# Kernel optimization log

Hardware: AMD Instinct MI355X
Metric: run time of the kernel (lower is better)

## Reference

```python
import jax, jax.numpy as jnp
import numpy as np

N_NODES = 100000
N_EDGES = 1600000
N_GRAPHS = 128
IN_F, H_F, OUT_F, HID, NCLS = 128, 128, 64, 10, 10

def setup_inputs() -> dict:
    key = jax.random.key(0)
    ks = jax.random.split(key, 12)
    feats = jax.random.normal(ks[0], (N_NODES, IN_F), dtype=jnp.float32)
    src = jax.random.randint(ks[1], (N_EDGES,), 0, N_NODES, dtype=jnp.int32)
    dst = jax.random.randint(ks[2], (N_EDGES,), 0, N_NODES, dtype=jnp.int32)
    graph_ids = jnp.sort(jax.random.randint(ks[3], (N_NODES,), 0, N_GRAPHS, dtype=jnp.int32))
    def glorot(k, shape):
        fan = shape[0] + shape[1]
        return jax.random.normal(k, shape, dtype=jnp.float32) * jnp.sqrt(2.0 / fan)
    return {
        'feats': feats, 'src': src, 'dst': dst, 'graph_ids': graph_ids,
        'W1': glorot(ks[4], (IN_F, H_F)), 'b1': jnp.zeros((H_F,), jnp.float32),
        'W2': glorot(ks[5], (H_F, OUT_F)), 'b2': jnp.zeros((OUT_F,), jnp.float32),
        'fcW1': glorot(ks[6], (OUT_F, HID)), 'fcb1': jnp.zeros((HID,), jnp.float32),
        'fcW2': glorot(ks[7], (HID, NCLS)), 'fcb2': jnp.zeros((NCLS,), jnp.float32),
    }

def _graph_conv(x, W, b, src, dst):
    # DGL GraphConv, norm='both': D_dst^{-1/2} A D_src^{-1/2} X W + b
    ones = jnp.ones((src.shape[0],), x.dtype)
    deg_out = jnp.clip(jax.ops.segment_sum(ones, src, num_segments=N_NODES), 1.0)
    deg_in = jnp.clip(jax.ops.segment_sum(ones, dst, num_segments=N_NODES), 1.0)
    x = x * jax.lax.rsqrt(deg_out)[:, None]
    m = jax.ops.segment_sum(x[src], dst, num_segments=N_NODES)  # gather-scatter over edges
    m = m * jax.lax.rsqrt(deg_in)[:, None]
    return m @ W + b

def reference(feats, src, dst, graph_ids, W1, b1, W2, b2, fcW1, fcb1, fcW2, fcb2):
    h = jax.nn.relu(_graph_conv(feats, W1, b1, src, dst))
    h = jax.nn.relu(_graph_conv(h, W2, b2, src, dst))
    # dgl.mean_nodes: per-graph mean pooling
    sums = jax.ops.segment_sum(h, graph_ids, num_segments=N_GRAPHS)
    counts = jnp.clip(jax.ops.segment_sum(jnp.ones((N_NODES,), h.dtype), graph_ids, num_segments=N_GRAPHS), 1.0)
    pooled = sums / counts[:, None]  # [G, OUT_F]
    z = jax.nn.relu(pooled @ fcW1 + fcb1)
    return jax.nn.softmax(z @ fcW2 + fcb2, axis=1)
```

## Files before the change

kernel.cpp:

```cpp
#include <hip/hip_runtime.h>
#include <hip/hip_bf16.h>

#define N_NODES 100000
#define N_EDGES 1600000
#define N_GRAPHS 128
#define IN_F 128
#define H_F 128
#define OUT_F 64
#define HID 10
#define NCLS 10
#define XPAD 136
#define BSH 7
#define NBUCK 782
#define SBLK 128
#define EPB (N_EDGES / SBLK)
#define NB_PREP 4
#define PCHUNK 8

typedef __attribute__((ext_vector_type(8))) short bf16x8;
typedef __attribute__((ext_vector_type(4))) float f32x4;
typedef __attribute__((ext_vector_type(2))) float f32x2;

__device__ __forceinline__ float bl(unsigned int u) { return __uint_as_float(u << 16); }
__device__ __forceinline__ float bh(unsigned int u) { return __uint_as_float(u & 0xffff0000u); }

__global__ __launch_bounds__(1024) void k_hist2(const int* __restrict__ src, const int* __restrict__ dst,
                                                int* __restrict__ Pd, int* __restrict__ Ps,
                                                const float* __restrict__ W1, const float* __restrict__ W2,
                                                unsigned short* __restrict__ Wt1, unsigned short* __restrict__ Wt2) {
    __shared__ int hd[NBUCK];
    __shared__ int hs[NBUCK];
    const int blk = blockIdx.x;
    if (blk < SBLK) {
        for (int i = threadIdx.x; i < NBUCK; i += 1024) { hd[i] = 0; hs[i] = 0; }
        __syncthreads();
        const int base = blk * EPB;
        for (int i = threadIdx.x; i < EPB; i += 1024) {
            atomicAdd(&hd[dst[base + i] >> BSH], 1);
            atomicAdd(&hs[src[base + i] >> BSH], 1);
        }
        __syncthreads();
        for (int b = threadIdx.x; b < NBUCK; b += 1024) {
            Pd[b * SBLK + blk] = hd[b];
            Ps[b * SBLK + blk] = hs[b];
        }
    } else {
        int t = (blk - SBLK) * 1024 + threadIdx.x;
        const int stride = NB_PREP * 1024;
        for (int i = t; i < 128 * 128; i += stride) {
            int c = i >> 7, k = i & 127;
            __hip_bfloat16 v = __float2bfloat16(W1[k * 128 + c]);
            Wt1[i] = *(unsigned short*)&v;
        }
        for (int i = t; i < 64 * 128; i += stride) {
            int c = i >> 7, k = i & 127;
            __hip_bfloat16 v = __float2bfloat16(W2[k * 64 + c]);
            Wt2[i] = *(unsigned short*)&v;
        }
    }
}

__global__ __launch_bounds__(128) void k_scanA(int* __restrict__ Pd, int* __restrict__ Ps,
                                               int* __restrict__ Td, int* __restrict__ Ts) {
    __shared__ int sc[128];
    const int b = blockIdx.x;
    const int t = threadIdx.x;
    int* P = (b < NBUCK) ? Pd : Ps;
    int* T = (b < NBUCK) ? Td : Ts;
    const int bb = (b < NBUCK) ? b : b - NBUCK;
    int v = P[bb * SBLK + t];
    sc[t] = v;
    __syncthreads();
    for (int off = 1; off < 128; off <<= 1) {
        int u = (t >= off) ? sc[t - off] : 0;
        __syncthreads();
        sc[t] += u;
        __syncthreads();
    }
    P[bb * SBLK + t] = sc[t] - v;
    if (t == 127) T[bb] = sc[127];
}

__global__ __launch_bounds__(1024) void k_scanB(const int* __restrict__ Td, const int* __restrict__ Ts,
                                                int* __restrict__ Bd, int* __restrict__ Bs) {
    __shared__ int sc[1024];
    const int t = threadIdx.x;
    int v = (t < NBUCK) ? Td[t] : 0;
    sc[t] = v;
    __syncthreads();
    for (int off = 1; off < 1024; off <<= 1) {
        int u = (t >= off) ? sc[t - off] : 0;
        __syncthreads();
        sc[t] += u;
        __syncthreads();
    }
    if (t < NBUCK) Bd[t] = sc[t] - v;
    if (t == NBUCK - 1) Bd[NBUCK] = sc[t];
    __syncthreads();
    int v2 = (t < NBUCK) ? Ts[t] : 0;
    sc[t] = v2;
    __syncthreads();
    for (int off = 1; off < 1024; off <<= 1) {
        int u = (t >= off) ? sc[t - off] : 0;
        __syncthreads();
        sc[t] += u;
        __syncthreads();
    }
    if (t < NBUCK) Bs[t] = sc[t] - v2;
    if (t == NBUCK - 1) Bs[NBUCK] = sc[t];
}

__global__ __launch_bounds__(1024) void k_scatter(const int* __restrict__ src, const int* __restrict__ dst,
                                                  const int* __restrict__ Pd, const int* __restrict__ Ps,
                                                  const int* __restrict__ Bd, const int* __restrict__ Bs,
                                                  unsigned int* __restrict__ pb, unsigned char* __restrict__ sb) {
    __shared__ int tk[NBUCK];
    const int b = blockIdx.x;
    const bool isPb = b < SBLK;
    const int blk = isPb ? b : b - SBLK;
    for (int i = threadIdx.x; i < NBUCK; i += 1024) tk[i] = 0;
    __syncthreads();
    const int base = blk * EPB;
    if (isPb) {
        for (int i = threadIdx.x; i < EPB; i += 1024) {
            int d = dst[base + i];
            int s = src[base + i];
            int bd = d >> BSH;
            int t = atomicAdd(&tk[bd], 1);
            pb[Bd[bd] + Pd[bd * SBLK + blk] + t] = ((unsigned)s << 7) | (unsigned)(d & 127);
        }
    } else {
        for (int i = threadIdx.x; i < EPB; i += 1024) {
            int s = src[base + i];
            int bs = s >> BSH;
            int t = atomicAdd(&tk[bs], 1);
            sb[Bs[bs] + Ps[bs * SBLK + blk] + t] = (unsigned char)(s & 127);
        }
    }
}

__global__ __launch_bounds__(256) void k_finalize(const unsigned int* __restrict__ pb, const int* __restrict__ Bd,
                                                  const unsigned char* __restrict__ sb, const int* __restrict__ Bs,
                                                  int* __restrict__ rp, int* __restrict__ cnt_out,
                                                  int* __restrict__ cols) {
    __shared__ int cnt[128];
    __shared__ int exc[128];
    __shared__ int tick[128];
    __shared__ int h[128];
    __shared__ int sc[128];
    const int b = blockIdx.x;
    const int tid = threadIdx.x;
    if (tid < 128) { cnt[tid] = 0; tick[tid] = 0; h[tid] = 0; }
    __syncthreads();
    const int e0 = Bd[b], e1 = Bd[b + 1];
    for (int i = e0 + tid; i < e1; i += 256) atomicAdd(&cnt[pb[i] & 127], 1);
    const int f0 = Bs[b], f1 = Bs[b + 1];
    for (int i = f0 + tid; i < f1; i += 256) atomicAdd(&h[sb[i]], 1);
    __syncthreads();
    if (tid < 128) sc[tid] = cnt[tid];
    __syncthreads();
    for (int off = 1; off < 128; off <<= 1) {
        int u = (tid < 128 && tid >= off) ? sc[tid - off] : 0;
        __syncthreads();
        if (tid < 128) sc[tid] += u;
        __syncthreads();
    }
    if (tid < 128) exc[tid] = sc[tid] - cnt[tid];
    __syncthreads();
    const int node0 = b << BSH;
    if (tid < 128 && node0 + tid < N_NODES) {
        rp[node0 + tid] = e0 + exc[tid];
        cnt_out[node0 + tid] = h[tid];
    }
    if (b == NBUCK - 1 && tid == 0) rp[N_NODES] = N_EDGES;
    for (int i = e0 + tid; i < e1; i += 256) {
        unsigned int p = pb[i];
        int loc = p & 127;
        int t = atomicAdd(&tick[loc], 1);
        cols[e0 + exc[loc] + t] = (int)(p >> 7);
    }
}

__global__ __launch_bounds__(256) void k_gemm1(const float* __restrict__ X,
                                               const unsigned short* __restrict__ Wt,
                                               const int* __restrict__ cnt_out,
                                               unsigned char* __restrict__ Gout) {
    __shared__ __align__(16) unsigned short Xs[32 * XPAD];
    __shared__ __align__(16) unsigned short Ws[128 * XPAD];
    const int tid = threadIdx.x;
    const int row0 = blockIdx.x * 32;

    {
        const float4* X4 = (const float4*)X;
#pragma unroll
        for (int j = 0; j < 4; j++) {
            int i = tid + 256 * j;
            int r = i >> 5, k4 = i & 31;
            float4 x = X4[(size_t)(row0 + r) * 32 + k4];
            __hip_bfloat162 lo = __float22bfloat162_rn({x.x, x.y});
            __hip_bfloat162 hi = __float22bfloat162_rn({x.z, x.w});
            uint2 u;
            u.x = *(unsigned int*)&lo;
            u.y = *(unsigned int*)&hi;
            *(uint2*)&Xs[r * XPAD + k4 * 4] = u;
        }
    }
    {
        const uint2* W2 = (const uint2*)Wt;
#pragma unroll
        for (int j = 0; j < 16; j++) {
            int i = tid + 256 * j;
            int cc = i >> 5, kk = i & 31;
            uint2 u = W2[(size_t)cc * 32 + kk];
            *(uint2*)&Ws[cc * XPAD + kk * 4] = u;
        }
    }
    __syncthreads();

    const int lane = tid & 63;
    const int wv = tid >> 6;
    const int m = lane & 15;
    const int q = lane >> 4;
    const int cg = wv * 32;

    f32x4 acc00 = {0.f, 0.f, 0.f, 0.f}, acc01 = {0.f, 0.f, 0.f, 0.f};
    f32x4 acc10 = {0.f, 0.f, 0.f, 0.f}, acc11 = {0.f, 0.f, 0.f, 0.f};
#pragma unroll
    for (int ks = 0; ks < 4; ks++) {
        int kb = ks * 32 + q * 8;
        bf16x8 a0 = *(const bf16x8*)&Xs[m * XPAD + kb];
        bf16x8 a1 = *(const bf16x8*)&Xs[(16 + m) * XPAD + kb];
        bf16x8 b0 = *(const bf16x8*)&Ws[(cg + m) * XPAD + kb];
        bf16x8 b1 = *(const bf16x8*)&Ws[(cg + 16 + m) * XPAD + kb];
        acc00 = __builtin_amdgcn_mfma_f32_16x16x32_bf16(a0, b0, acc00, 0, 0, 0);
        acc01 = __builtin_amdgcn_mfma_f32_16x16x32_bf16(a0, b1, acc01, 0, 0, 0);
        acc10 = __builtin_amdgcn_mfma_f32_16x16x32_bf16(a1, b0, acc10, 0, 0, 0);
        acc11 = __builtin_amdgcn_mfma_f32_16x16x32_bf16(a1, b1, acc11, 0, 0, 0);
    }
#pragma unroll
    for (int r = 0; r < 4; r++) {
        int rowA = row0 + q * 4 + r;
        int rowB = rowA + 16;
        float sA = rsqrtf((float)max(cnt_out[rowA], 1));
        float sB = rsqrtf((float)max(cnt_out[rowB], 1));
        unsigned int pkA = __builtin_amdgcn_cvt_pk_fp8_f32(acc00[r] * sA, acc01[r] * sA, 0, false);
        unsigned int pkB = __builtin_amdgcn_cvt_pk_fp8_f32(acc10[r] * sB, acc11[r] * sB, 0, false);
        unsigned char* gA = Gout + (size_t)rowA * 128 + cg + m;
        gA[0]  = (unsigned char)(pkA & 0xffu);
        gA[16] = (unsigned char)((pkA >> 8) & 0xffu);
        unsigned char* gB = Gout + (size_t)rowB * 128 + cg + m;
        gB[0]  = (unsigned char)(pkB & 0xffu);
        gB[16] = (unsigned char)((pkB >> 8) & 0xffu);
    }
}

template <int TOTF, bool XBF16, bool OUT_FP8>
__global__ __launch_bounds__(256) void k_gemm_mfma(const void* __restrict__ Xv,
                                                   const unsigned short* __restrict__ Wt,
                                                   const int* __restrict__ cnt_out,
                                                   void* __restrict__ GoutV) {
    __shared__ __align__(16) unsigned short Xs[32 * XPAD];
    __shared__ __align__(16) unsigned short Ws[64 * XPAD];
    const int tid = threadIdx.x;
    const int cbase = blockIdx.y * 64;
    const int row0 = blockIdx.x * 32;

    if constexpr (XBF16) {
        const uint2* X2 = (const uint2*)Xv;
#pragma unroll
        for (int j = 0; j < 4; j++) {
            int i = tid + 256 * j;
            int r = i >> 5, kk = i & 31;
            uint2 u = X2[(size_t)(row0 + r) * 32 + kk];
            *(uint2*)&Xs[r * XPAD + kk * 4] = u;
        }
    } else {
        const float4* X4 = (const float4*)Xv;
#pragma unroll
        for (int j = 0; j < 4; j++) {
            int i = tid + 256 * j;
            int r = i >> 5, k4 = i & 31;
            float4 x = X4[(size_t)(row0 + r) * 32 + k4];
            __hip_bfloat162 lo = __float22bfloat162_rn({x.x, x.y});
            __hip_bfloat162 hi = __float22bfloat162_rn({x.z, x.w});
            uint2 u;
            u.x = *(unsigned int*)&lo;
            u.y = *(unsigned int*)&hi;
            *(uint2*)&Xs[r * XPAD + k4 * 4] = u;
        }
    }
    {
        const uint2* W2 = (const uint2*)Wt;
#pragma unroll
        for (int j = 0; j < 8; j++) {
            int i = tid + 256 * j;
            int c = i >> 5, kk = i & 31;
            uint2 u = W2[(size_t)(cbase + c) * 32 + kk];
            *(uint2*)&Ws[c * XPAD + kk * 4] = u;
        }
    }
    __syncthreads();

    const int lane = tid & 63;
    const int wv = tid >> 6;
    const int m = lane & 15;
    const int q = lane >> 4;
    const int roff = (wv & 1) * 16;
    const int coff = (wv >> 1) * 32;

    f32x4 acc0 = {0.f, 0.f, 0.f, 0.f}, acc1 = {0.f, 0.f, 0.f, 0.f};
#pragma unroll
    for (int ks = 0; ks < 4; ks++) {
        int kb = ks * 32 + q * 8;
        bf16x8 a  = *(const bf16x8*)&Xs[(roff + m) * XPAD + kb];
        bf16x8 b0 = *(const bf16x8*)&Ws[(coff + m) * XPAD + kb];
        bf16x8 b1 = *(const bf16x8*)&Ws[(coff + 16 + m) * XPAD + kb];
        acc0 = __builtin_amdgcn_mfma_f32_16x16x32_bf16(a, b0, acc0, 0, 0, 0);
        acc1 = __builtin_amdgcn_mfma_f32_16x16x32_bf16(a, b1, acc1, 0, 0, 0);
    }
#pragma unroll
    for (int r = 0; r < 4; r++) {
        int row = row0 + roff + q * 4 + r;
        float s = rsqrtf((float)max(cnt_out[row], 1));
        int col0 = cbase + coff + m;
        if constexpr (OUT_FP8) {
            unsigned int pk = __builtin_amdgcn_cvt_pk_fp8_f32(acc0[r] * s, acc1[r] * s, 0, false);
            unsigned char* gp = (unsigned char*)GoutV + (size_t)row * TOTF + col0;
            gp[0]  = (unsigned char)(pk & 0xffu);
            gp[16] = (unsigned char)((pk >> 8) & 0xffu);
        } else {
            unsigned short* Gout = (unsigned short*)GoutV;
            __hip_bfloat16 o0 = __float2bfloat16(acc0[r] * s);
            __hip_bfloat16 o1 = __float2bfloat16(acc1[r] * s);
            Gout[(size_t)row * TOTF + col0]      = *(unsigned short*)&o0;
            Gout[(size_t)row * TOTF + col0 + 16] = *(unsigned short*)&o1;
        }
    }
}

__device__ __forceinline__ void acc8(uint2 u, f32x2& a01, f32x2& a23, f32x2& a45, f32x2& a67) {
    a01 += __builtin_amdgcn_cvt_pk_f32_fp8(u.x, false);
    a23 += __builtin_amdgcn_cvt_pk_f32_fp8(u.x, true);
    a45 += __builtin_amdgcn_cvt_pk_f32_fp8(u.y, false);
    a67 += __builtin_amdgcn_cvt_pk_f32_fp8(u.y, true);
}
__device__ __forceinline__ float red2(float x) {
    x += __shfl_xor(x, 16);
    x += __shfl_xor(x, 32);
    return x;
}

__global__ __launch_bounds__(256) void k_spmm128f8(const unsigned int* __restrict__ G,
                                                   const int* __restrict__ rp,
                                                   const int* __restrict__ cols,
                                                   const float* __restrict__ bias,
                                                   uint4* __restrict__ H4) {
    const int lane = threadIdx.x & 63;
    const int wave = threadIdx.x >> 6;
    const int v = blockIdx.x * 4 + wave;
    const int b0 = rp[v];
    const int deg = rp[v + 1] - b0;
    const int c = lane & 15;
    const int h = lane >> 4;
    const uint2* G2 = (const uint2*)G;
    f32x2 a01 = {0.f, 0.f}, a23 = {0.f, 0.f}, a45 = {0.f, 0.f}, a67 = {0.f, 0.f};
    for (int base = 0; base < deg; base += 64) {
        const int n = min(64, deg - base);
        const int mycol = (lane < n) ? cols[b0 + base + lane] : 0;
        const int n16 = n & ~15;
        for (int j = 0; j < n16; j += 16) {
            int s0 = __shfl(mycol, j + h);
            int s1 = __shfl(mycol, j + 4 + h);
            int s2 = __shfl(mycol, j + 8 + h);
            int s3 = __shfl(mycol, j + 12 + h);
            uint2 u0 = G2[(size_t)s0 * 16 + c];
            uint2 u1 = G2[(size_t)s1 * 16 + c];
            uint2 u2 = G2[(size_t)s2 * 16 + c];
            uint2 u3 = G2[(size_t)s3 * 16 + c];
            acc8(u0, a01, a23, a45, a67);
            acc8(u1, a01, a23, a45, a67);
            acc8(u2, a01, a23, a45, a67);
            acc8(u3, a01, a23, a45, a67);
        }
        for (int j = n16; j < n; j += 4) {
            int idx = j + h;
            int sj = __shfl(mycol, min(idx, n - 1));
            if (idx < n) {
                uint2 u = G2[(size_t)sj * 16 + c];
                acc8(u, a01, a23, a45, a67);
            }
        }
    }
    float r0 = red2(a01.x), r1 = red2(a01.y), r2 = red2(a23.x), r3 = red2(a23.y);
    float r4 = red2(a45.x), r5 = red2(a45.y), r6 = red2(a67.x), r7 = red2(a67.y);
    if (h == 0) {
        float rs = rsqrtf((float)max(deg, 1));
        float4 bA = *(const float4*)&bias[8 * c];
        float4 bB = *(const float4*)&bias[8 * c + 4];
        __hip_bfloat162 p0 = __float22bfloat162_rn({fmaxf(fmaf(r0, rs, bA.x), 0.f),
                                                    fmaxf(fmaf(r1, rs, bA.y), 0.f)});
        __hip_bfloat162 p1 = __float22bfloat162_rn({fmaxf(fmaf(r2, rs, bA.z), 0.f),
                                                    fmaxf(fmaf(r3, rs, bA.w), 0.f)});
        __hip_bfloat162 p2 = __float22bfloat162_rn({fmaxf(fmaf(r4, rs, bB.x), 0.f),
                                                    fmaxf(fmaf(r5, rs, bB.y), 0.f)});
        __hip_bfloat162 p3 = __float22bfloat162_rn({fmaxf(fmaf(r6, rs, bB.z), 0.f),
                                                    fmaxf(fmaf(r7, rs, bB.w), 0.f)});
        uint4 o;
        o.x = *(unsigned int*)&p0;
        o.y = *(unsigned int*)&p1;
        o.z = *(unsigned int*)&p2;
        o.w = *(unsigned int*)&p3;
        H4[(size_t)v * 16 + c] = o;
    }
}

__global__ __launch_bounds__(256) void k_spmm64f8(const unsigned int* __restrict__ G,
                                                  const int* __restrict__ rp,
                                                  const int* __restrict__ cols,
                                                  const float* __restrict__ bias,
                                                  uint2* __restrict__ H2) {
    const int lane = threadIdx.x & 63;
    const int wave = threadIdx.x >> 6;
    const int v = blockIdx.x * 4 + wave;
    const int b0 = rp[v];
    const int deg = rp[v + 1] - b0;
    const int c = lane & 15;
    const int h = lane >> 4;
    f32x2 a01 = {0.f, 0.f}, a23 = {0.f, 0.f};
    for (int base = 0; base < deg; base += 64) {
        const int n = min(64, deg - base);
        const int mycol = (lane < n) ? cols[b0 + base + lane] : 0;
        const int n16 = n & ~15;
        for (int j = 0; j < n16; j += 16) {
            int s0 = __shfl(mycol, j + h);
            int s1 = __shfl(mycol, j + 4 + h);
            int s2 = __shfl(mycol, j + 8 + h);
            int s3 = __shfl(mycol, j + 12 + h);
            unsigned int u0 = G[(size_t)s0 * 16 + c];
            unsigned int u1 = G[(size_t)s1 * 16 + c];
            unsigned int u2 = G[(size_t)s2 * 16 + c];
            unsigned int u3 = G[(size_t)s3 * 16 + c];
            a01 += __builtin_amdgcn_cvt_pk_f32_fp8(u0, false);
            a23 += __builtin_amdgcn_cvt_pk_f32_fp8(u0, true);
            a01 += __builtin_amdgcn_cvt_pk_f32_fp8(u1, false);
            a23 += __builtin_amdgcn_cvt_pk_f32_fp8(u1, true);
            a01 += __builtin_amdgcn_cvt_pk_f32_fp8(u2, false);
            a23 += __builtin_amdgcn_cvt_pk_f32_fp8(u2, true);
            a01 += __builtin_amdgcn_cvt_pk_f32_fp8(u3, false);
            a23 += __builtin_amdgcn_cvt_pk_f32_fp8(u3, true);
        }
        for (int j = n16; j < n; j += 4) {
            int idx = j + h;
            int sj = __shfl(mycol, min(idx, n - 1));
            if (idx < n) {
                unsigned int u = G[(size_t)sj * 16 + c];
                a01 += __builtin_amdgcn_cvt_pk_f32_fp8(u, false);
                a23 += __builtin_amdgcn_cvt_pk_f32_fp8(u, true);
            }
        }
    }
    float ax = red2(a01.x), ay = red2(a01.y), az = red2(a23.x), aw = red2(a23.y);
    if (h == 0) {
        float r = rsqrtf((float)max(deg, 1));
        float4 b = *(const float4*)&bias[4 * c];
        __hip_bfloat162 p0 = __float22bfloat162_rn({fmaxf(fmaf(ax, r, b.x), 0.f),
                                                    fmaxf(fmaf(ay, r, b.y), 0.f)});
        __hip_bfloat162 p1 = __float22bfloat162_rn({fmaxf(fmaf(az, r, b.z), 0.f),
                                                    fmaxf(fmaf(aw, r, b.w), 0.f)});
        uint2 o;
        o.x = *(unsigned int*)&p0;
        o.y = *(unsigned int*)&p1;
        H2[(size_t)v * 16 + c] = o;
    }
}

__global__ __launch_bounds__(256) void k_pool(const unsigned short* __restrict__ h2,
                                              const int* __restrict__ gid,
                                              float* __restrict__ part) {
    __shared__ int se[2];
    __shared__ float red[16][16][4];
    const int cpart = blockIdx.x;
    const int g = blockIdx.y;
    const int tid = threadIdx.x;
    if (tid < 2) {
        int target = g + tid;
        int lo = 0, hi = N_NODES;
        while (lo < hi) {
            int mid = (lo + hi) >> 1;
            if (gid[mid] < target) lo = mid + 1; else hi = mid;
        }
        se[tid] = lo;
    }
    __syncthreads();
    const int s = se[0], e = se[1];
    const int chunk = (e - s + PCHUNK - 1) / PCHUNK;
    const int lo = s + cpart * chunk;
    const int hi = min(lo + chunk, e);
    const int r = tid >> 4, cp = tid & 15;
    float a0 = 0.f, a1 = 0.f, a2 = 0.f, a3 = 0.f;
    const uint2* H = (const uint2*)h2;
    for (int v = lo + r; v < hi; v += 16) {
        uint2 u = H[(size_t)v * 16 + cp];
        a0 += bl(u.x); a1 += bh(u.x); a2 += bl(u.y); a3 += bh(u.y);
    }
    red[r][cp][0] = a0; red[r][cp][1] = a1; red[r][cp][2] = a2; red[r][cp][3] = a3;
    for (int off = 8; off > 0; off >>= 1) {
        __syncthreads();
        if (r < off) {
#pragma unroll
            for (int k = 0; k < 4; k++) red[r][cp][k] += red[r + off][cp][k];
        }
    }
    __syncthreads();
    if (r == 0) {
        float4 o = {red[0][cp][0], red[0][cp][1], red[0][cp][2], red[0][cp][3]};
        *(float4*)&part[((size_t)cpart * N_GRAPHS + g) * 64 + 4 * cp] = o;
    }
}

__global__ __launch_bounds__(64) void k_mlp(const float* __restrict__ part,
                                            const int* __restrict__ gid,
                                            const float* __restrict__ fcW1,
                                            const float* __restrict__ fcb1,
                                            const float* __restrict__ fcW2,
                                            const float* __restrict__ fcb2,
                                            float* __restrict__ out) {
    __shared__ int se[2];
    __shared__ float p[64];
    __shared__ float z[10];
    __shared__ float l[10];
    __shared__ float red[2];
    const int g = blockIdx.x;
    const int t = threadIdx.x;
    if (t < 2) {
        int target = g + t;
        int lo = 0, hi = N_NODES;
        while (lo < hi) {
            int mid = (lo + hi) >> 1;
            if (gid[mid] < target) lo = mid + 1; else hi = mid;
        }
        se[t] = lo;
    }
    __syncthreads();
    const int cnt = max(se[1] - se[0], 1);
    float a = 0.f;
#pragma unroll
    for (int c = 0; c < PCHUNK; c++) a += part[((size_t)c * N_GRAPHS + g) * 64 + t];
    p[t] = a / (float)cnt;
    __syncthreads();
    if (t < 10) {
        float acc = fcb1[t];
        for (int k = 0; k < 64; k++) acc = fmaf(p[k], fcW1[k * 10 + t], acc);
        z[t] = fmaxf(acc, 0.f);
    }
    __syncthreads();
    if (t < 10) {
        float acc = fcb2[t];
        for (int k = 0; k < 10; k++) acc = fmaf(z[k], fcW2[k * 10 + t], acc);
        l[t] = acc;
    }
    __syncthreads();
    if (t == 0) {
        float m = l[0];
        for (int i = 1; i < 10; i++) m = fmaxf(m, l[i]);
        float ssum = 0.f;
        for (int i = 0; i < 10; i++) ssum += expf(l[i] - m);
        red[0] = m;
        red[1] = ssum;
    }
    __syncthreads();
    if (t < 10) out[g * 10 + t] = expf(l[t] - red[0]) / red[1];
}

extern "C" void kernel_launch(void* const* d_in, const int* in_sizes, int n_in,
                              void* d_out, int out_size, void* d_ws, size_t ws_size,
                              hipStream_t stream) {
    const float* feats = (const float*)d_in[0];
    const int* src = (const int*)d_in[1];
    const int* dst = (const int*)d_in[2];
    const int* gid = (const int*)d_in[3];
    const float* W1 = (const float*)d_in[4];
    const float* b1 = (const float*)d_in[5];
    const float* W2 = (const float*)d_in[6];
    const float* b2 = (const float*)d_in[7];
    const float* fcW1 = (const float*)d_in[8];
    const float* fcb1 = (const float*)d_in[9];
    const float* fcW2 = (const float*)d_in[10];
    const float* fcb2 = (const float*)d_in[11];
    float* out = (float*)d_out;

    char* w = (char*)d_ws;
    size_t off = 0;
    auto alloc = [&](size_t bytes) -> void* {
        void* p = w + off;
        off = (off + bytes + 255) & ~(size_t)255;
        return p;
    };
    int* cnt_out = (int*)alloc(N_NODES * 4);
    int* rp      = (int*)alloc((N_NODES + 1) * 4);
    int* cols    = (int*)alloc((size_t)N_EDGES * 4);
    int* Pd      = (int*)alloc(NBUCK * SBLK * 4);
    int* Ps      = (int*)alloc(NBUCK * SBLK * 4);
    int* Td      = (int*)alloc(NBUCK * 4);
    int* Ts      = (int*)alloc(NBUCK * 4);
    int* Bd      = (int*)alloc((NBUCK + 1) * 4);
    int* Bs      = (int*)alloc((NBUCK + 1) * 4);
    unsigned int* pb  = (unsigned int*)alloc((size_t)N_EDGES * 4);
    unsigned char* sb = (unsigned char*)alloc((size_t)N_EDGES);
    unsigned short* Wt1 = (unsigned short*)alloc(128 * 128 * 2);
    unsigned short* Wt2 = (unsigned short*)alloc(64 * 128 * 2);
    unsigned char* g1 = (unsigned char*)alloc((size_t)N_NODES * 128);
    unsigned short* h1 = (unsigned short*)alloc((size_t)N_NODES * 128 * 2);
    unsigned char* g2 = (unsigned char*)alloc((size_t)N_NODES * 64);
    unsigned short* h2 = (unsigned short*)alloc((size_t)N_NODES * 64 * 2);
    float* part = (float*)alloc((size_t)PCHUNK * N_GRAPHS * 64 * 4);

    k_hist2<<<SBLK + NB_PREP, 1024, 0, stream>>>(src, dst, Pd, Ps, W1, W2, Wt1, Wt2);
    k_scanA<<<2 * NBUCK, 128, 0, stream>>>(Pd, Ps, Td, Ts);
    k_scanB<<<1, 1024, 0, stream>>>(Td, Ts, Bd, Bs);
    k_scatter<<<2 * SBLK, 1024, 0, stream>>>(src, dst, Pd, Ps, Bd, Bs, pb, sb);
    k_finalize<<<NBUCK, 256, 0, stream>>>(pb, Bd, sb, Bs, rp, cnt_out, cols);

    k_gemm1<<<N_NODES / 32, 256, 0, stream>>>(feats, Wt1, cnt_out, g1);
    k_spmm128f8<<<N_NODES / 4, 256, 0, stream>>>((const unsigned int*)g1, rp, cols, b1, (uint4*)h1);

    k_gemm_mfma<64, true, true><<<dim3(N_NODES / 32, 1), 256, 0, stream>>>(h1, Wt2, cnt_out, g2);
    k_spmm64f8<<<N_NODES / 4, 256, 0, stream>>>((const unsigned int*)g2, rp, cols, b2, (uint2*)h2);

    k_pool<<<dim3(PCHUNK, N_GRAPHS), 256, 0, stream>>>(h2, gid, part);
    k_mlp<<<N_GRAPHS, 64, 0, stream>>>(part, gid, fcW1, fcb1, fcW2, fcb2, out);
}
```

Baseline: 287.9 us.

## Process eight nodes per wave in SpMM with double-buffered neighbor gathers

```diff
diff --git a/kernel.cpp b/kernel.cpp
--- a/kernel.cpp
+++ b/kernel.cpp
@@ -344,35 +344,62 @@
     a45 += __builtin_amdgcn_cvt_pk_f32_fp8(u.y, false);
     a67 += __builtin_amdgcn_cvt_pk_f32_fp8(u.y, true);
 }
+__device__ __forceinline__ void acc4(unsigned int u, f32x2& a01, f32x2& a23) {
+    a01 += __builtin_amdgcn_cvt_pk_f32_fp8(u, false);
+    a23 += __builtin_amdgcn_cvt_pk_f32_fp8(u, true);
+}
 __device__ __forceinline__ float red2(float x) {
     x += __shfl_xor(x, 16);
     x += __shfl_xor(x, 32);
     return x;
 }
 
-__global__ __launch_bounds__(256) void k_spmm128f8(const unsigned int* __restrict__ G,
-                                                   const int* __restrict__ rp,
-                                                   const int* __restrict__ cols,
-                                                   const float* __restrict__ bias,
-                                                   uint4* __restrict__ H4) {
-    const int lane = threadIdx.x & 63;
-    const int wave = threadIdx.x >> 6;
-    const int v = blockIdx.x * 4 + wave;
-    const int b0 = rp[v];
-    const int deg = rp[v + 1] - b0;
-    const int c = lane & 15;
-    const int h = lane >> 4;
-    const uint2* G2 = (const uint2*)G;
-    f32x2 a01 = {0.f, 0.f}, a23 = {0.f, 0.f}, a45 = {0.f, 0.f}, a67 = {0.f, 0.f};
-    for (int base = 0; base < deg; base += 64) {
-        const int n = min(64, deg - base);
-        const int mycol = (lane < n) ? cols[b0 + base + lane] : 0;
-        const int n16 = n & ~15;
+
+__device__ __forceinline__ void gat128(const uint2* __restrict__ G2, int mycol, int nr, int c, int h,
+                                       uint2 (&u)[8]) {
+#pragma unroll
+    for (int s = 0; s < 8; s++)
+        if (4 * s < nr) {
+            int row = __shfl(mycol, 4 * s + h);
+            u[s] = G2[(size_t)row * 16 + c];
+        }
+}
+__device__ __forceinline__ void acc128(const uint2 (&u)[8], int nr, int h,
+                                       f32x2& a01, f32x2& a23, f32x2& a45, f32x2& a67) {
+#pragma unroll
+    for (int s = 0; s < 8; s++) {
+        if (4 * s + 4 <= nr) {
+            acc8(u[s], a01, a23, a45, a67);
+        } else if (4 * s < nr) {
+            bool ok = (4 * s + h) < nr;
+            uint2 uu;
+            uu.x = ok ? u[s].x : 0u;
+            uu.y = ok ? u[s].y : 0u;
+            acc8(uu, a01, a23, a45, a67);
+        }
+    }
+}
+__device__ __forceinline__ void slow128(const uint2* __restrict__ G2, const int* __restrict__ cols,
+                                        int b0, int d, int mycol, int lane, int c, int h,
+                                        f32x2& a01, f32x2& a23, f32x2& a45, f32x2& a67) {
+    const int n = min(d, 64);
+    for (int j = 32; j < n; j += 4) {
+        int idx = j + h;
+        int sj = __shfl(mycol, min(idx, n - 1));
+        if (idx < n) {
+            uint2 uu = G2[(size_t)sj * 16 + c];
+            acc8(uu, a01, a23, a45, a67);
+        }
+    }
+    for (int base = 64; base < d; base += 64) {
+        const int nn = min(64, d - base);
+        const int mc2 = (lane < nn) ? cols[b0 + base + lane] : 0;
+        const int n16 = nn & ~15;
         for (int j = 0; j < n16; j += 16) {
-            int s0 = __shfl(mycol, j + h);
-            int s1 = __shfl(mycol, j + 4 + h);
-            int s2 = __shfl(mycol, j + 8 + h);
-            int s3 = __shfl(mycol, j + 12 + h);
+            int s0 = __shfl(mc2, j + h);
+            int s1 = __shfl(mc2, j + 4 + h);
+            int s2 = __shfl(mc2, j + 8 + h);
+            int s3 = __shfl(mc2, j + 12 + h);
             uint2 u0 = G2[(size_t)s0 * 16 + c];
             uint2 u1 = G2[(size_t)s1 * 16 + c];
             uint2 u2 = G2[(size_t)s2 * 16 + c];
@@ -382,15 +409,19 @@
             acc8(u2, a01, a23, a45, a67);
             acc8(u3, a01, a23, a45, a67);
         }
-        for (int j = n16; j < n; j += 4) {
+        for (int j = n16; j < nn; j += 4) {
             int idx = j + h;
-            int sj = __shfl(mycol, min(idx, n - 1));
-            if (idx < n) {
-                uint2 u = G2[(size_t)sj * 16 + c];
-                acc8(u, a01, a23, a45, a67);
+            int sj = __shfl(mc2, min(idx, nn - 1));
+            if (idx < nn) {
+                uint2 uu = G2[(size_t)sj * 16 + c];
+                acc8(uu, a01, a23, a45, a67);
             }
         }
     }
+}
+__device__ __forceinline__ void store128(uint4* __restrict__ H4, const float* __restrict__ bias,
+                                         int v, int deg, int c, int h,
+                                         f32x2 a01, f32x2 a23, f32x2 a45, f32x2 a67) {
     float r0 = red2(a01.x), r1 = red2(a01.y), r2 = red2(a23.x), r3 = red2(a23.y);
     float r4 = red2(a45.x), r5 = red2(a45.y), r6 = red2(a67.x), r7 = red2(a67.y);
     if (h == 0) {
@@ -414,6 +445,131 @@
     }
 }
 
+__global__ __launch_bounds__(256) void k_spmm128f8(const unsigned int* __restrict__ G,
+                                                   const int* __restrict__ rp,
+                                                   const int* __restrict__ cols,
+                                                   const float* __restrict__ bias,
+                                                   uint4* __restrict__ H4) {
+    const int lane = threadIdx.x & 63;
+    const int wave = threadIdx.x >> 6;
+    const int v0 = (blockIdx.x * 4 + wave) * 8;
+    const int c = lane & 15;
+    const int h = lane >> 4;
+    const uint2* G2 = (const uint2*)G;
+
+    int rpl = (lane < 9) ? rp[v0 + lane] : 0;
+    int rv[9];
+#pragma unroll
+    for (int t = 0; t < 9; t++) rv[t] = __builtin_amdgcn_readfirstlane(__shfl(rpl, t));
+    int b[8], d[8];
+#pragma unroll
+    for (int i = 0; i < 8; i++) { b[i] = rv[i]; d[i] = rv[i + 1] - rv[i]; }
+
+    uint2 u[2][2][8];
+    int mc[2][2];
+    mc[0][0] = (lane < d[0]) ? cols[b[0] + lane] : 0;
+    mc[0][1] = (lane < d[1]) ? cols[b[1] + lane] : 0;
+    mc[1][0] = (lane < d[2]) ? cols[b[2] + lane] : 0;
+    mc[1][1] = (lane < d[3]) ? cols[b[3] + lane] : 0;
+    gat128(G2, mc[0][0], min(d[0], 32), c, h, u[0][0]);
+    gat128(G2, mc[0][1], min(d[1], 32), c, h, u[0][1]);
+
+#pragma unroll
+    for (int p = 0; p < 4; p++) {
+        const int par = p & 1, nxt = par ^ 1;
+        const int i0 = 2 * p, i1 = 2 * p + 1;
+        if (p < 3) {
+            gat128(G2, mc[nxt][0], min(d[i0 + 2], 32), c, h, u[nxt][0]);
+            gat128(G2, mc[nxt][1], min(d[i0 + 3], 32), c, h, u[nxt][1]);
+        }
+        f32x2 a01 = {0.f, 0.f}, a23 = {0.f, 0.f}, a45 = {0.f, 0.f}, a67 = {0.f, 0.f};
+        acc128(u[par][0], min(d[i0], 32), h, a01, a23, a45, a67);
+        if (d[i0] > 32) slow128(G2, cols, b[i0], d[i0], mc[par][0], lane, c, h, a01, a23, a45, a67);
+        f32x2 c01 = {0.f, 0.f}, c23 = {0.f, 0.f}, c45 = {0.f, 0.f}, c67 = {0.f, 0.f};
+        acc128(u[par][1], min(d[i1], 32), h, c01, c23, c45, c67);
+        if (d[i1] > 32) slow128(G2, cols, b[i1], d[i1], mc[par][1], lane, c, h, c01, c23, c45, c67);
+        if (p < 2) {
+            mc[par][0] = (lane < d[i0 + 4]) ? cols[b[i0 + 4] + lane] : 0;
+            mc[par][1] = (lane < d[i0 + 5]) ? cols[b[i0 + 5] + lane] : 0;
+        }
+        store128(H4, bias, v0 + i0, d[i0], c, h, a01, a23, a45, a67);
+        store128(H4, bias, v0 + i1, d[i1], c, h, c01, c23, c45, c67);
+    }
+}
+
+
+__device__ __forceinline__ void gat64(const unsigned int* __restrict__ G, int mycol, int nr, int c, int h,
+                                      unsigned int (&u)[8]) {
+#pragma unroll
+    for (int s = 0; s < 8; s++)
+        if (4 * s < nr) {
+            int row = __shfl(mycol, 4 * s + h);
+            u[s] = G[(size_t)row * 16 + c];
+        }
+}
+__device__ __forceinline__ void acc64s(const unsigned int (&u)[8], int nr, int h,
+                                       f32x2& a01, f32x2& a23) {
+#pragma unroll
+    for (int s = 0; s < 8; s++) {
+        if (4 * s + 4 <= nr) {
+            acc4(u[s], a01, a23);
+        } else if (4 * s < nr) {
+            bool ok = (4 * s + h) < nr;
+            acc4(ok ? u[s] : 0u, a01, a23);
+        }
+    }
+}
+__device__ __forceinline__ void slow64(const unsigned int* __restrict__ G, const int* __restrict__ cols,
+                                       int b0, int d, int mycol, int lane, int c, int h,
+                                       f32x2& a01, f32x2& a23) {
+    const int n = min(d, 64);
+    for (int j = 32; j < n; j += 4) {
+        int idx = j + h;
+        int sj = __shfl(mycol, min(idx, n - 1));
+        if (idx < n) acc4(G[(size_t)sj * 16 + c], a01, a23);
+    }
+    for (int base = 64; base < d; base += 64) {
+        const int nn = min(64, d - base);
+        const int mc2 = (lane < nn) ? cols[b0 + base + lane] : 0;
+        const int n16 = nn & ~15;
+        for (int j = 0; j < n16; j += 16) {
+            int s0 = __shfl(mc2, j + h);
+            int s1 = __shfl(mc2, j + 4 + h);
+            int s2 = __shfl(mc2, j + 8 + h);
+            int s3 = __shfl(mc2, j + 12 + h);
+            unsigned int u0 = G[(size_t)s0 * 16 + c];
+            unsigned int u1 = G[(size_t)s1 * 16 + c];
+            unsigned int u2 = G[(size_t)s2 * 16 + c];
+            unsigned int u3 = G[(size_t)s3 * 16 + c];
+            acc4(u0, a01, a23);
+            acc4(u1, a01, a23);
+            acc4(u2, a01, a23);
+            acc4(u3, a01, a23);
+        }
+        for (int j = n16; j < nn; j += 4) {
+            int idx = j + h;
+            int sj = __shfl(mc2, min(idx, nn - 1));
+            if (idx < nn) acc4(G[(size_t)sj * 16 + c], a01, a23);
+        }
+    }
+}
+__device__ __forceinline__ void store64(uint2* __restrict__ H2, const float* __restrict__ bias,
+                                        int v, int deg, int c, int h, f32x2 a01, f32x2 a23) {
+    float ax = red2(a01.x), ay = red2(a01.y), az = red2(a23.x), aw = red2(a23.y);
+    if (h == 0) {
+        float r = rsqrtf((float)max(deg, 1));
+        float4 bb = *(const float4*)&bias[4 * c];
+        __hip_bfloat162 p0 = __float22bfloat162_rn({fmaxf(fmaf(ax, r, bb.x), 0.f),
+                                                    fmaxf(fmaf(ay, r, bb.y), 0.f)});
+        __hip_bfloat162 p1 = __float22bfloat162_rn({fmaxf(fmaf(az, r, bb.z), 0.f),
+                                                    fmaxf(fmaf(aw, r, bb.w), 0.f)});
+        uint2 o;
+        o.x = *(unsigned int*)&p0;
+        o.y = *(unsigned int*)&p1;
+        H2[(size_t)v * 16 + c] = o;
+    }
+}
+
 __global__ __launch_bounds__(256) void k_spmm64f8(const unsigned int* __restrict__ G,
                                                   const int* __restrict__ rp,
                                                   const int* __restrict__ cols,
@@ -421,56 +577,47 @@
                                                   uint2* __restrict__ H2) {
     const int lane = threadIdx.x & 63;
     const int wave = threadIdx.x >> 6;
-    const int v = blockIdx.x * 4 + wave;
-    const int b0 = rp[v];
-    const int deg = rp[v + 1] - b0;
+    const int v0 = (blockIdx.x * 4 + wave) * 8;
     const int c = lane & 15;
     const int h = lane >> 4;
-    f32x2 a01 = {0.f, 0.f}, a23 = {0.f, 0.f};
-    for (int base = 0; base < deg; base += 64) {
-        const int n = min(64, deg - base);
-        const int mycol = (lane < n) ? cols[b0 + base + lane] : 0;
-        const int n16 = n & ~15;
-        for (int j = 0; j < n16; j += 16) {
-            int s0 = __shfl(mycol, j + h);
-            int s1 = __shfl(mycol, j + 4 + h);
-            int s2 = __shfl(mycol, j + 8 + h);
-            int s3 = __shfl(mycol, j + 12 + h);
-            unsigned int u0 = G[(size_t)s0 * 16 + c];
-            unsigned int u1 = G[(size_t)s1 * 16 + c];
-            unsigned int u2 = G[(size_t)s2 * 16 + c];
-            unsigned int u3 = G[(size_t)s3 * 16 + c];
-            a01 += __builtin_amdgcn_cvt_pk_f32_fp8(u0, false);
-            a23 += __builtin_amdgcn_cvt_pk_f32_fp8(u0, true);
-            a01 += __builtin_amdgcn_cvt_pk_f32_fp8(u1, false);
-            a23 += __builtin_amdgcn_cvt_pk_f32_fp8(u1, true);
-            a01 += __builtin_amdgcn_cvt_pk_f32_fp8(u2, false);
-            a23 += __builtin_amdgcn_cvt_pk_f32_fp8(u2, true);
-            a01 += __builtin_amdgcn_cvt_pk_f32_fp8(u3, false);
-            a23 += __builtin_amdgcn_cvt_pk_f32_fp8(u3, true);
-        }
-        for (int j = n16; j < n; j += 4) {
-            int idx = j + h;
-            int sj = __shfl(mycol, min(idx, n - 1));
-            if (idx < n) {
-                unsigned int u = G[(size_t)sj * 16 + c];
-                a01 += __builtin_amdgcn_cvt_pk_f32_fp8(u, false);
-                a23 += __builtin_amdgcn_cvt_pk_f32_fp8(u, true);
-            }
-        }
-    }
-    float ax = red2(a01.x), ay = red2(a01.y), az = red2(a23.x), aw = red2(a23.y);
-    if (h == 0) {
-        float r = rsqrtf((float)max(deg, 1));
-        float4 b = *(const float4*)&bias[4 * c];
-        __hip_bfloat162 p0 = __float22bfloat162_rn({fmaxf(fmaf(ax, r, b.x), 0.f),
-                                                    fmaxf(fmaf(ay, r, b.y), 0.f)});
-        __hip_bfloat162 p1 = __float22bfloat162_rn({fmaxf(fmaf(az, r, b.z), 0.f),
-                                                    fmaxf(fmaf(aw, r, b.w), 0.f)});
-        uint2 o;
-        o.x = *(unsigned int*)&p0;
-        o.y = *(unsigned int*)&p1;
-        H2[(size_t)v * 16 + c] = o;
+
+    int rpl = (lane < 9) ? rp[v0 + lane] : 0;
+    int rv[9];
+#pragma unroll
+    for (int t = 0; t < 9; t++) rv[t] = __builtin_amdgcn_readfirstlane(__shfl(rpl, t));
+    int b[8], d[8];
+#pragma unroll
+    for (int i = 0; i < 8; i++) { b[i] = rv[i]; d[i] = rv[i + 1] - rv[i]; }
+
+    unsigned int u[2][2][8];
+    int mc[2][2];
+    mc[0][0] = (lane < d[0]) ? cols[b[0] + lane] : 0;
+    mc[0][1] = (lane < d[1]) ? cols[b[1] + lane] : 0;
+    mc[1][0] = (lane < d[2]) ? cols[b[2] + lane] : 0;
+    mc[1][1] = (lane < d[3]) ? cols[b[3] + lane] : 0;
+    gat64(G, mc[0][0], min(d[0], 32), c, h, u[0][0]);
+    gat64(G, mc[0][1], min(d[1], 32), c, h, u[0][1]);
+
+#pragma unroll
+    for (int p = 0; p < 4; p++) {
+        const int par = p & 1, nxt = par ^ 1;
+        const int i0 = 2 * p, i1 = 2 * p + 1;
+        if (p < 3) {
+            gat64(G, mc[nxt][0], min(d[i0 + 2], 32), c, h, u[nxt][0]);
+            gat64(G, mc[nxt][1], min(d[i0 + 3], 32), c, h, u[nxt][1]);
+        }
+        f32x2 a01 = {0.f, 0.f}, a23 = {0.f, 0.f};
+        acc64s(u[par][0], min(d[i0], 32), h, a01, a23);
+        if (d[i0] > 32) slow64(G, cols, b[i0], d[i0], mc[par][0], lane, c, h, a01, a23);
+        f32x2 c01 = {0.f, 0.f}, c23 = {0.f, 0.f};
+        acc64s(u[par][1], min(d[i1], 32), h, c01, c23);
+        if (d[i1] > 32) slow64(G, cols, b[i1], d[i1], mc[par][1], lane, c, h, c01, c23);
+        if (p < 2) {
+            mc[par][0] = (lane < d[i0 + 4]) ? cols[b[i0 + 4] + lane] : 0;
+            mc[par][1] = (lane < d[i0 + 5]) ? cols[b[i0 + 5] + lane] : 0;
+        }
+        store64(H2, bias, v0 + i0, d[i0], c, h, a01, a23);
+        store64(H2, bias, v0 + i1, d[i1], c, h, c01, c23);
     }
 }
 
@@ -622,10 +769,10 @@
     k_finalize<<<NBUCK, 256, 0, stream>>>(pb, Bd, sb, Bs, rp, cnt_out, cols);
 
     k_gemm1<<<N_NODES / 32, 256, 0, stream>>>(feats, Wt1, cnt_out, g1);
-    k_spmm128f8<<<N_NODES / 4, 256, 0, stream>>>((const unsigned int*)g1, rp, cols, b1, (uint4*)h1);
+    k_spmm128f8<<<N_NODES / 32, 256, 0, stream>>>((const unsigned int*)g1, rp, cols, b1, (uint4*)h1);
 
     k_gemm_mfma<64, true, true><<<dim3(N_NODES / 32, 1), 256, 0, stream>>>(h1, Wt2, cnt_out, g2);
-    k_spmm64f8<<<N_NODES / 4, 256, 0, stream>>>((const unsigned int*)g2, rp, cols, b2, (uint2*)h2);
+    k_spmm64f8<<<N_NODES / 32, 256, 0, stream>>>((const unsigned int*)g2, rp, cols, b2, (uint2*)h2);
 
     k_pool<<<dim3(PCHUNK, N_GRAPHS), 256, 0, stream>>>(h2, gid, part);
     k_mlp<<<N_GRAPHS, 64, 0, stream>>>(part, gid, fcW1, fcb1, fcW2, fcb2, out);
```

Result: slower. 333.5 us (+15.8%).

## Remap SpMM gathers so each wave walks edges serially across all feature lanes

Applied to the files above, without the earlier changes.

```diff
diff --git a/kernel.cpp b/kernel.cpp
--- a/kernel.cpp
+++ b/kernel.cpp
@@ -338,140 +338,125 @@
     }
 }
 
-__device__ __forceinline__ void acc8(uint2 u, f32x2& a01, f32x2& a23, f32x2& a45, f32x2& a67) {
-    a01 += __builtin_amdgcn_cvt_pk_f32_fp8(u.x, false);
-    a23 += __builtin_amdgcn_cvt_pk_f32_fp8(u.x, true);
-    a45 += __builtin_amdgcn_cvt_pk_f32_fp8(u.y, false);
-    a67 += __builtin_amdgcn_cvt_pk_f32_fp8(u.y, true);
-}
-__device__ __forceinline__ float red2(float x) {
-    x += __shfl_xor(x, 16);
-    x += __shfl_xor(x, 32);
-    return x;
-}
-
-__global__ __launch_bounds__(256) void k_spmm128f8(const unsigned int* __restrict__ G,
+__global__ __launch_bounds__(256) void k_spmm128f8(const unsigned short* __restrict__ G,
                                                    const int* __restrict__ rp,
                                                    const int* __restrict__ cols,
                                                    const float* __restrict__ bias,
-                                                   uint4* __restrict__ H4) {
+                                                   unsigned int* __restrict__ H) {
     const int lane = threadIdx.x & 63;
     const int wave = threadIdx.x >> 6;
     const int v = blockIdx.x * 4 + wave;
-    const int b0 = rp[v];
-    const int deg = rp[v + 1] - b0;
-    const int c = lane & 15;
-    const int h = lane >> 4;
-    const uint2* G2 = (const uint2*)G;
-    f32x2 a01 = {0.f, 0.f}, a23 = {0.f, 0.f}, a45 = {0.f, 0.f}, a67 = {0.f, 0.f};
-    for (int base = 0; base < deg; base += 64) {
-        const int n = min(64, deg - base);
-        const int mycol = (lane < n) ? cols[b0 + base + lane] : 0;
-        const int n16 = n & ~15;
-        for (int j = 0; j < n16; j += 16) {
-            int s0 = __shfl(mycol, j + h);
-            int s1 = __shfl(mycol, j + 4 + h);
-            int s2 = __shfl(mycol, j + 8 + h);
-            int s3 = __shfl(mycol, j + 12 + h);
-            uint2 u0 = G2[(size_t)s0 * 16 + c];
-            uint2 u1 = G2[(size_t)s1 * 16 + c];
-            uint2 u2 = G2[(size_t)s2 * 16 + c];
-            uint2 u3 = G2[(size_t)s3 * 16 + c];
-            acc8(u0, a01, a23, a45, a67);
-            acc8(u1, a01, a23, a45, a67);
-            acc8(u2, a01, a23, a45, a67);
-            acc8(u3, a01, a23, a45, a67);
-        }
-        for (int j = n16; j < n; j += 4) {
-            int idx = j + h;
-            int sj = __shfl(mycol, min(idx, n - 1));
-            if (idx < n) {
-                uint2 u = G2[(size_t)sj * 16 + c];
-                acc8(u, a01, a23, a45, a67);
-            }
-        }
-    }
-    float r0 = red2(a01.x), r1 = red2(a01.y), r2 = red2(a23.x), r3 = red2(a23.y);
-    float r4 = red2(a45.x), r5 = red2(a45.y), r6 = red2(a67.x), r7 = red2(a67.y);
-    if (h == 0) {
-        float rs = rsqrtf((float)max(deg, 1));
-        float4 bA = *(const float4*)&bias[8 * c];
-        float4 bB = *(const float4*)&bias[8 * c + 4];
-        __hip_bfloat162 p0 = __float22bfloat162_rn({fmaxf(fmaf(r0, rs, bA.x), 0.f),
-                                                    fmaxf(fmaf(r1, rs, bA.y), 0.f)});
-        __hip_bfloat162 p1 = __float22bfloat162_rn({fmaxf(fmaf(r2, rs, bA.z), 0.f),
-                                                    fmaxf(fmaf(r3, rs, bA.w), 0.f)});
-        __hip_bfloat162 p2 = __float22bfloat162_rn({fmaxf(fmaf(r4, rs, bB.x), 0.f),
-                                                    fmaxf(fmaf(r5, rs, bB.y), 0.f)});
-        __hip_bfloat162 p3 = __float22bfloat162_rn({fmaxf(fmaf(r6, rs, bB.z), 0.f),
-                                                    fmaxf(fmaf(r7, rs, bB.w), 0.f)});
-        uint4 o;
-        o.x = *(unsigned int*)&p0;
-        o.y = *(unsigned int*)&p1;
-        o.z = *(unsigned int*)&p2;
-        o.w = *(unsigned int*)&p3;
-        H4[(size_t)v * 16 + c] = o;
-    }
-}
-
-__global__ __launch_bounds__(256) void k_spmm64f8(const unsigned int* __restrict__ G,
+    const int b0 = __builtin_amdgcn_readfirstlane(rp[v]);
+    const int e0 = __builtin_amdgcn_readfirstlane(rp[v + 1]);
+    const int deg = e0 - b0;
+    const unsigned short* gl = G + lane;
+    f32x2 acc = {0.f, 0.f};
+    int j = 0;
+    while (j + 16 <= deg) {
+        unsigned int u[16];
+#pragma unroll
+        for (int k = 0; k < 16; k++) {
+            int s = cols[b0 + j + k];
+            u[k] = gl[(size_t)s * 64];
+        }
+#pragma unroll
+        for (int k = 0; k < 16; k++) acc += __builtin_amdgcn_cvt_pk_f32_fp8(u[k], false);
+        j += 16;
+    }
+    if (j + 8 <= deg) {
+        unsigned int u[8];
+#pragma unroll
+        for (int k = 0; k < 8; k++) { int s = cols[b0 + j + k]; u[k] = gl[(size_t)s * 64]; }
+#pragma unroll
+        for (int k = 0; k < 8; k++) acc += __builtin_amdgcn_cvt_pk_f32_fp8(u[k], false);
+        j += 8;
+    }
+    if (j + 4 <= deg) {
+        unsigned int u[4];
+#pragma unroll
+        for (int k = 0; k < 4; k++) { int s = cols[b0 + j + k]; u[k] = gl[(size_t)s * 64]; }
+#pragma unroll
+        for (int k = 0; k < 4; k++) acc += __builtin_amdgcn_cvt_pk_f32_fp8(u[k], false);
+        j += 4;
+    }
+    if (j + 2 <= deg) {
+        unsigned int u0, u1;
+        { int s = cols[b0 + j];     u0 = gl[(size_t)s * 64]; }
+        { int s = cols[b0 + j + 1]; u1 = gl[(size_t)s * 64]; }
+        acc += __builtin_amdgcn_cvt_pk_f32_fp8(u0, false);
+        acc += __builtin_amdgcn_cvt_pk_f32_fp8(u1, false);
+        j += 2;
+    }
+    if (j < deg) {
+        int s = cols[b0 + j];
+        unsigned int u = gl[(size_t)s * 64];
+        acc += __builtin_amdgcn_cvt_pk_f32_fp8(u, false);
+    }
+    const float rs = rsqrtf((float)max(deg, 1));
+    const float2 bb = *(const float2*)&bias[2 * lane];
+    __hip_bfloat162 p = __float22bfloat162_rn({fmaxf(fmaf(acc.x, rs, bb.x), 0.f),
+                                               fmaxf(fmaf(acc.y, rs, bb.y), 0.f)});
+    H[(size_t)v * 64 + lane] = *(unsigned int*)&p;
+}
+
+__global__ __launch_bounds__(256) void k_spmm64f8(const unsigned char* __restrict__ G,
                                                   const int* __restrict__ rp,
                                                   const int* __restrict__ cols,
                                                   const float* __restrict__ bias,
-                                                  uint2* __restrict__ H2) {
+                                                  unsigned short* __restrict__ H) {
     const int lane = threadIdx.x & 63;
     const int wave = threadIdx.x >> 6;
     const int v = blockIdx.x * 4 + wave;
-    const int b0 = rp[v];
-    const int deg = rp[v + 1] - b0;
-    const int c = lane & 15;
-    const int h = lane >> 4;
-    f32x2 a01 = {0.f, 0.f}, a23 = {0.f, 0.f};
-    for (int base = 0; base < deg; base += 64) {
-        const int n = min(64, deg - base);
-        const int mycol = (lane < n) ? cols[b0 + base + lane] : 0;
-        const int n16 = n & ~15;
-        for (int j = 0; j < n16; j += 16) {
-            int s0 = __shfl(mycol, j + h);
-            int s1 = __shfl(mycol, j + 4 + h);
-            int s2 = __shfl(mycol, j + 8 + h);
-            int s3 = __shfl(mycol, j + 12 + h);
-            unsigned int u0 = G[(size_t)s0 * 16 + c];
-            unsigned int u1 = G[(size_t)s1 * 16 + c];
-            unsigned int u2 = G[(size_t)s2 * 16 + c];
-            unsigned int u3 = G[(size_t)s3 * 16 + c];
-            a01 += __builtin_amdgcn_cvt_pk_f32_fp8(u0, false);
-            a23 += __builtin_amdgcn_cvt_pk_f32_fp8(u0, true);
-            a01 += __builtin_amdgcn_cvt_pk_f32_fp8(u1, false);
-            a23 += __builtin_amdgcn_cvt_pk_f32_fp8(u1, true);
-            a01 += __builtin_amdgcn_cvt_pk_f32_fp8(u2, false);
-            a23 += __builtin_amdgcn_cvt_pk_f32_fp8(u2, true);
-            a01 += __builtin_amdgcn_cvt_pk_f32_fp8(u3, false);
-            a23 += __builtin_amdgcn_cvt_pk_f32_fp8(u3, true);
-        }
-        for (int j = n16; j < n; j += 4) {
-            int idx = j + h;
-            int sj = __shfl(mycol, min(idx, n - 1));
-            if (idx < n) {
-                unsigned int u = G[(size_t)sj * 16 + c];
-                a01 += __builtin_amdgcn_cvt_pk_f32_fp8(u, false);
-                a23 += __builtin_amdgcn_cvt_pk_f32_fp8(u, true);
-            }
-        }
-    }
-    float ax = red2(a01.x), ay = red2(a01.y), az = red2(a23.x), aw = red2(a23.y);
-    if (h == 0) {
-        float r = rsqrtf((float)max(deg, 1));
-        float4 b = *(const float4*)&bias[4 * c];
-        __hip_bfloat162 p0 = __float22bfloat162_rn({fmaxf(fmaf(ax, r, b.x), 0.f),
-                                                    fmaxf(fmaf(ay, r, b.y), 0.f)});
-        __hip_bfloat162 p1 = __float22bfloat162_rn({fmaxf(fmaf(az, r, b.z), 0.f),
-                                                    fmaxf(fmaf(aw, r, b.w), 0.f)});
-        uint2 o;
-        o.x = *(unsigned int*)&p0;
-        o.y = *(unsigned int*)&p1;
-        H2[(size_t)v * 16 + c] = o;
-    }
+    const int b0 = __builtin_amdgcn_readfirstlane(rp[v]);
+    const int e0 = __builtin_amdgcn_readfirstlane(rp[v + 1]);
+    const int deg = e0 - b0;
+    const unsigned char* gl = G + lane;
+    f32x2 acc = {0.f, 0.f};
+    int j = 0;
+    while (j + 16 <= deg) {
+        unsigned int u[16];
+#pragma unroll
+        for (int k = 0; k < 16; k++) {
+            int s = cols[b0 + j + k];
+            u[k] = gl[(size_t)s * 64];
+        }
+#pragma unroll
+        for (int k = 0; k < 16; k++) acc += __builtin_amdgcn_cvt_pk_f32_fp8(u[k], false);
+        j += 16;
+    }
+    if (j + 8 <= deg) {
+        unsigned int u[8];
+#pragma unroll
+        for (int k = 0; k < 8; k++) { int s = cols[b0 + j + k]; u[k] = gl[(size_t)s * 64]; }
+#pragma unroll
+        for (int k = 0; k < 8; k++) acc += __builtin_amdgcn_cvt_pk_f32_fp8(u[k], false);
+        j += 8;
+    }
+    if (j + 4 <= deg) {
+        unsigned int u[4];
+#pragma unroll
+        for (int k = 0; k < 4; k++) { int s = cols[b0 + j + k]; u[k] = gl[(size_t)s * 64]; }
+#pragma unroll
+        for (int k = 0; k < 4; k++) acc += __builtin_amdgcn_cvt_pk_f32_fp8(u[k], false);
+        j += 4;
+    }
+    if (j + 2 <= deg) {
+        unsigned int u0, u1;
+        { int s = cols[b0 + j];     u0 = gl[(size_t)s * 64]; }
+        { int s = cols[b0 + j + 1]; u1 = gl[(size_t)s * 64]; }
+        acc += __builtin_amdgcn_cvt_pk_f32_fp8(u0, false);
+        acc += __builtin_amdgcn_cvt_pk_f32_fp8(u1, false);
+        j += 2;
+    }
+    if (j < deg) {
+        int s = cols[b0 + j];
+        unsigned int u = gl[(size_t)s * 64];
+        acc += __builtin_amdgcn_cvt_pk_f32_fp8(u, false);
+    }
+    const float rs = rsqrtf((float)max(deg, 1));
+    const float b = bias[lane];
+    __hip_bfloat16 o = __float2bfloat16(fmaxf(fmaf(acc.x, rs, b), 0.f));
+    H[(size_t)v * 64 + lane] = *(unsigned short*)&o;
 }
 
 __global__ __launch_bounds__(256) void k_pool(const unsigned short* __restrict__ h2,
@@ -622,10 +607,10 @@
     k_finalize<<<NBUCK, 256, 0, stream>>>(pb, Bd, sb, Bs, rp, cnt_out, cols);
 
     k_gemm1<<<N_NODES / 32, 256, 0, stream>>>(feats, Wt1, cnt_out, g1);
-    k_spmm128f8<<<N_NODES / 4, 256, 0, stream>>>((const unsigned int*)g1, rp, cols, b1, (uint4*)h1);
+    k_spmm128f8<<<N_NODES / 4, 256, 0, stream>>>((const unsigned short*)g1, rp, cols, b1, (unsigned int*)h1);
 
     k_gemm_mfma<64, true, true><<<dim3(N_NODES / 32, 1), 256, 0, stream>>>(h1, Wt2, cnt_out, g2);
-    k_spmm64f8<<<N_NODES / 4, 256, 0, stream>>>((const unsigned int*)g2, rp, cols, b2, (uint2*)h2);
+    k_spmm64f8<<<N_NODES / 4, 256, 0, stream>>>(g2, rp, cols, b2, (unsigned short*)h2);
 
     k_pool<<<dim3(PCHUNK, N_GRAPHS), 256, 0, stream>>>(h2, gid, part);
     k_mlp<<<N_GRAPHS, 64, 0, stream>>>(part, gid, fcW1, fcb1, fcW2, fcb2, out);
```

Result: faster. 279.7 us (-2.9%).
